# Kernel tuning notes

Hardware: AMD Instinct MI355X
Metric: run time of the kernel (lower is better)

## Reference

```python
import jax, jax.numpy as jnp
from jax import lax
import numpy as np

N_LAYER = 2
SEQ, BATCH, D = 4096, 32, 512


def setup_inputs() -> dict:
    key = jax.random.key(0)
    k1, k2, k3 = jax.random.split(key, 3)
    x = jax.random.normal(k1, (SEQ, BATCH, D), dtype=jnp.float32)
    # repo init: weight_ih ~ N(0, 0.01)
    W_ih = jax.random.normal(k2, (N_LAYER, D, D), dtype=jnp.float32) * 0.01
    # recurrent weight in [0,1) keeps the long ReLU recurrence bounded
    w_hh = jax.random.uniform(k3, (N_LAYER, D), dtype=jnp.float32)
    b_ih = jnp.zeros((N_LAYER, D), dtype=jnp.float32)
    return {"x": x, "W_ih": W_ih, "w_hh": w_hh, "b_ih": b_ih}


def _indrnn_layer(x, W, w, b):
    # x: (T, B, in), W: (H, in), w,b: (H,)
    proj = jnp.einsum('tbi,hi->tbh', x, W) + b  # one batched GEMM up front

    def step(h, p):
        h = jax.nn.relu(p + w * h)
        return h, h

    h0 = jnp.zeros((x.shape[1], W.shape[0]), dtype=x.dtype)
    hT, ys = lax.scan(step, h0, proj)
    return ys, hT


def reference(x, W_ih, w_hh, b_ih):
    hiddens = []
    out = x
    for l in range(W_ih.shape[0]):  # small fixed layer loop
        out, hT = _indrnn_layer(out, W_ih[l], w_hh[l], b_ih[l])
        hiddens.append(hT)
    h_n = jnp.stack(hiddens, axis=0)  # (n_layer, B, H)
    return out, h_n
```

## Files before the change

kernel.cpp:

```cpp
#include <hip/hip_runtime.h>

#define T_SEQ   4096
#define BATCH   32
#define DIM     512
#define MROWS   (T_SEQ * BATCH)
#define S_STRIDE (BATCH * DIM)
#define OUT_ELEMS ((size_t)T_SEQ * BATCH * DIM)
#define NCH     32
#define CLEN    (T_SEQ / NCH)
#define NCHAIN  (BATCH * DIM)
#define NWG     ((MROWS / 128) * (DIM / 128))

typedef __bf16 bf8_t __attribute__((ext_vector_type(8)));
typedef float  f4_t  __attribute__((ext_vector_type(4)));
typedef unsigned short u16x8 __attribute__((ext_vector_type(8)));
typedef __attribute__((address_space(1))) void gvoid_t;
typedef __attribute__((address_space(3))) void lvoid_t;

__device__ __forceinline__ unsigned short f2bf(float f) {
    unsigned int u = __float_as_uint(f);
    u += 0x7FFFu + ((u >> 16) & 1u);
    return (unsigned short)(u >> 16);
}
__device__ __forceinline__ float bf2f(unsigned short b) {
    return __uint_as_float(((unsigned int)b) << 16);
}

__global__ __launch_bounds__(256) void k_cvt(const float* __restrict__ in,
                                             unsigned short* __restrict__ out) {
    size_t i = ((size_t)blockIdx.x * 256 + threadIdx.x) * 8;
    float4 a = *reinterpret_cast<const float4*>(in + i);
    float4 b = *reinterpret_cast<const float4*>(in + i + 4);
    u16x8 o;
    o[0] = f2bf(a.x); o[1] = f2bf(a.y); o[2] = f2bf(a.z); o[3] = f2bf(a.w);
    o[4] = f2bf(b.x); o[5] = f2bf(b.y); o[6] = f2bf(b.z); o[7] = f2bf(b.w);
    *reinterpret_cast<u16x8*>(out + i) = o;
}

template <int AF32>
__global__ __launch_bounds__(256)
void k_gemm_bt(const void* __restrict__ Ap,
               const unsigned short* __restrict__ B,
               unsigned short* __restrict__ C) {
    __shared__ unsigned short As[128 * 32];
    __shared__ unsigned short Bs[128 * 32];

    const int tid  = threadIdx.x;
    const int lane = tid & 63;
    const int wv   = tid >> 6;
    const int wr   = wv >> 1;
    const int wc   = wv & 1;

    const int flat = blockIdx.x;
    const int s    = (flat & 7) * (NWG / 8) + (flat >> 3);
    const size_t gm = (size_t)(s >> 2) * 128;
    const int    gn = (s & 3) * 128;

    const int srow = tid >> 2;
    const int skk  = (tid & 3) * 8;

    f4_t acc[4][4] = {};

    const int l15 = lane & 15;
    const int lk  = (lane >> 4) * 8;

    for (int k0 = 0; k0 < 512; k0 += 32) {
#pragma unroll
        for (int i = 0; i < 2; ++i) {
            const unsigned short* gb = B + (size_t)(gn + i * 64 + srow) * 512 + k0 + skk;
            __builtin_amdgcn_global_load_lds((gvoid_t*)gb, (lvoid_t*)&Bs[i * 2048 + wv * 512], 16, 0, 0);
            if constexpr (AF32) {
                const float* ga = (const float*)Ap + (gm + (size_t)(i * 64 + srow)) * 512 + k0 + skk;
                float4 a0 = *reinterpret_cast<const float4*>(ga);
                float4 a1 = *reinterpret_cast<const float4*>(ga + 4);
                u16x8 o;
                o[0] = f2bf(a0.x); o[1] = f2bf(a0.y); o[2] = f2bf(a0.z); o[3] = f2bf(a0.w);
                o[4] = f2bf(a1.x); o[5] = f2bf(a1.y); o[6] = f2bf(a1.z); o[7] = f2bf(a1.w);
                *reinterpret_cast<u16x8*>(&As[i * 2048 + tid * 8]) = o;
            } else {
                const unsigned short* ga = (const unsigned short*)Ap + (gm + (size_t)(i * 64 + srow)) * 512 + k0 + skk;
                __builtin_amdgcn_global_load_lds((gvoid_t*)ga, (lvoid_t*)&As[i * 2048 + wv * 512], 16, 0, 0);
            }
        }
        __syncthreads();

        bf8_t af[4], bfz[4];
#pragma unroll
        for (int m = 0; m < 4; ++m)
            af[m] = *reinterpret_cast<const bf8_t*>(&As[(wr * 64 + m * 16 + l15) * 32 + lk]);
#pragma unroll
        for (int n = 0; n < 4; ++n)
            bfz[n] = *reinterpret_cast<const bf8_t*>(&Bs[(wc * 64 + n * 16 + l15) * 32 + lk]);
#pragma unroll
        for (int m = 0; m < 4; ++m)
#pragma unroll
            for (int n = 0; n < 4; ++n)
                acc[m][n] = __builtin_amdgcn_mfma_f32_16x16x32_bf16(af[m], bfz[n], acc[m][n], 0, 0, 0);
        __syncthreads();
    }

    const int crow0 = (lane >> 4) * 4;
#pragma unroll
    for (int m = 0; m < 4; ++m)
#pragma unroll
        for (int n = 0; n < 4; ++n) {
            const size_t row0 = gm + (size_t)(wr * 64 + m * 16 + crow0);
            const int    col  = gn + wc * 64 + n * 16 + l15;
#pragma unroll
            for (int r = 0; r < 4; ++r)
                C[(row0 + r) * 512 + col] = f2bf(acc[m][n][r]);
        }
}

__global__ __launch_bounds__(256)
void k_scan_p1(const unsigned short* __restrict__ q,
               const float* __restrict__ w_hh,
               const float* __restrict__ b_ih,
               float* __restrict__ Asum,
               float* __restrict__ Bsum) {
    const int g = (blockIdx.x & 63) * 256 + threadIdx.x;
    const int c = blockIdx.x >> 6;
    const float w  = w_hh[g & 511];
    const float bs = b_ih[g & 511];
    const unsigned short* p = q + (size_t)c * CLEN * S_STRIDE + g;

    float A = 0.f, Bv = 0.f;
    float s0[8], s1[8];
#pragma unroll
    for (int j = 0; j < 8; ++j) s0[j] = bf2f(p[(size_t)j * S_STRIDE]);
#pragma unroll
    for (int j = 0; j < 8; ++j) s1[j] = bf2f(p[(size_t)(8 + j) * S_STRIDE]);

    for (int j0 = 0; j0 < CLEN; j0 += 16) {
#pragma unroll
        for (int j = 0; j < 8; ++j) {
            float qv = s0[j] + bs;
            A  = fmaxf(fmaf(w, A, qv), 0.f);
            Bv = fmaf(w, Bv, qv);
        }
        if (j0 + 16 < CLEN) {
#pragma unroll
            for (int j = 0; j < 8; ++j) s0[j] = bf2f(p[(size_t)(j0 + 16 + j) * S_STRIDE]);
        }
#pragma unroll
        for (int j = 0; j < 8; ++j) {
            float qv = s1[j] + bs;
            A  = fmaxf(fmaf(w, A, qv), 0.f);
            Bv = fmaf(w, Bv, qv);
        }
        if (j0 + 24 < CLEN) {
#pragma unroll
            for (int j = 0; j < 8; ++j) s1[j] = bf2f(p[(size_t)(j0 + 24 + j) * S_STRIDE]);
        }
    }
    Asum[(size_t)c * NCHAIN + g] = A;
    Bsum[(size_t)c * NCHAIN + g] = Bv;
}

template <int MODE>
__global__ __launch_bounds__(256)
void k_scan_p2(const unsigned short* __restrict__ q,
               const float* __restrict__ w_hh,
               const float* __restrict__ b_ih,
               const float* __restrict__ Asum,
               const float* __restrict__ Bsum,
               float* __restrict__ of32,
               unsigned short* __restrict__ ob16,
               float* __restrict__ hT) {
    const int g = (blockIdx.x & 63) * 256 + threadIdx.x;
    const int c = blockIdx.x >> 6;
    const float w  = w_hh[g & 511];
    const float bs = b_ih[g & 511];

    float cw = w;
#pragma unroll
    for (int i = 0; i < 7; ++i) cw *= cw;
    float h = 0.f;
    for (int cc = 0; cc < c; ++cc)
        h = fmaxf(Asum[(size_t)cc * NCHAIN + g], fmaf(cw, h, Bsum[(size_t)cc * NCHAIN + g]));

    const size_t base = (size_t)c * CLEN * S_STRIDE + g;
    const unsigned short* p = q + base;

    float s0[8], s1[8];
#pragma unroll
    for (int j = 0; j < 8; ++j) s0[j] = bf2f(p[(size_t)j * S_STRIDE]);
#pragma unroll
    for (int j = 0; j < 8; ++j) s1[j] = bf2f(p[(size_t)(8 + j) * S_STRIDE]);

    for (int j0 = 0; j0 < CLEN; j0 += 16) {
#pragma unroll
        for (int j = 0; j < 8; ++j) {
            h = fmaxf(fmaf(w, h, s0[j] + bs), 0.f);
            const size_t idx = base + (size_t)(j0 + j) * S_STRIDE;
            if (MODE == 0) of32[idx] = h; else ob16[idx] = f2bf(h);
        }
        if (j0 + 16 < CLEN) {
#pragma unroll
            for (int j = 0; j < 8; ++j) s0[j] = bf2f(p[(size_t)(j0 + 16 + j) * S_STRIDE]);
        }
#pragma unroll
        for (int j = 0; j < 8; ++j) {
            h = fmaxf(fmaf(w, h, s1[j] + bs), 0.f);
            const size_t idx = base + (size_t)(j0 + 8 + j) * S_STRIDE;
            if (MODE == 0) of32[idx] = h; else ob16[idx] = f2bf(h);
        }
        if (j0 + 24 < CLEN) {
#pragma unroll
            for (int j = 0; j < 8; ++j) s1[j] = bf2f(p[(size_t)(j0 + 24 + j) * S_STRIDE]);
        }
    }
    if (c == NCH - 1) hT[g] = h;
}

extern "C" void kernel_launch(void* const* d_in, const int* in_sizes, int n_in,
                              void* d_out, int out_size, void* d_ws, size_t ws_size,
                              hipStream_t stream) {
    const float* x    = (const float*)d_in[0];
    const float* W_ih = (const float*)d_in[1];
    const float* w_hh = (const float*)d_in[2];
    const float* b_ih = (const float*)d_in[3];

    unsigned short* proj2 = (unsigned short*)d_ws;
    unsigned short* Wb    = proj2 + OUT_ELEMS;
    float* Asum = (float*)(Wb + 2 * 512 * 512);
    float* Bsum = Asum + (size_t)NCH * NCHAIN;

    unsigned short* proj1 = (unsigned short*)d_out;
    unsigned short* ys1   = proj1 + OUT_ELEMS;
    float* out = (float*)d_out;
    float* hT  = out + OUT_ELEMS;

    const int sgrid = 64 * NCH;

    k_cvt<<<524288 / 8 / 256, 256, 0, stream>>>(W_ih, Wb);
    k_gemm_bt<1><<<NWG, 256, 0, stream>>>(x, Wb, proj1);
    k_scan_p1<<<sgrid, 256, 0, stream>>>(proj1, w_hh, b_ih, Asum, Bsum);
    k_scan_p2<1><<<sgrid, 256, 0, stream>>>(proj1, w_hh, b_ih, Asum, Bsum,
                                            nullptr, ys1, hT);
    k_gemm_bt<0><<<NWG, 256, 0, stream>>>(ys1, Wb + 512 * 512, proj2);
    k_scan_p1<<<sgrid, 256, 0, stream>>>(proj2, w_hh + DIM, b_ih + DIM, Asum, Bsum);
    k_scan_p2<0><<<sgrid, 256, 0, stream>>>(proj2, w_hh + DIM, b_ih + DIM, Asum, Bsum,
                                            out, nullptr, hT + NCHAIN);
}
```

Baseline: 469.1 us.

## Keep weight tile in registers with persistent streaming GEMM over row chunks

```diff
diff --git a/kernel.cpp b/kernel.cpp
--- a/kernel.cpp
+++ b/kernel.cpp
@@ -9,7 +9,10 @@
 #define NCH     32
 #define CLEN    (T_SEQ / NCH)
 #define NCHAIN  (BATCH * DIM)
-#define NWG     ((MROWS / 128) * (DIM / 128))
+
+#define CHROWS  32
+#define NCHUNK  16
+#define LDSB    98304
 
 typedef __bf16 bf8_t __attribute__((ext_vector_type(8)));
 typedef float  f4_t  __attribute__((ext_vector_type(4)));
@@ -26,90 +29,134 @@
     return __uint_as_float(((unsigned int)b) << 16);
 }
 
-__global__ __launch_bounds__(256) void k_cvt(const float* __restrict__ in,
-                                             unsigned short* __restrict__ out) {
-    size_t i = ((size_t)blockIdx.x * 256 + threadIdx.x) * 8;
-    float4 a = *reinterpret_cast<const float4*>(in + i);
-    float4 b = *reinterpret_cast<const float4*>(in + i + 4);
-    u16x8 o;
-    o[0] = f2bf(a.x); o[1] = f2bf(a.y); o[2] = f2bf(a.z); o[3] = f2bf(a.w);
-    o[4] = f2bf(b.x); o[5] = f2bf(b.y); o[6] = f2bf(b.z); o[7] = f2bf(b.w);
-    *reinterpret_cast<u16x8*>(out + i) = o;
-}
+#define VMCn(n) asm volatile("s_waitcnt vmcnt(" #n ")" ::: "memory")
+#define LGKM0   asm volatile("s_waitcnt lgkmcnt(0)" ::: "memory")
 
 template <int AF32>
-__global__ __launch_bounds__(256)
-void k_gemm_bt(const void* __restrict__ Ap,
-               const unsigned short* __restrict__ B,
+__global__ __launch_bounds__(256, 1)
+void k_gemm_bs(const void* __restrict__ Ap,
+               const float* __restrict__ Bf,
                unsigned short* __restrict__ C) {
-    __shared__ unsigned short As[128 * 32];
-    __shared__ unsigned short Bs[128 * 32];
+    extern __shared__ unsigned short lds[];
 
     const int tid  = threadIdx.x;
     const int lane = tid & 63;
     const int wv   = tid >> 6;
-    const int wr   = wv >> 1;
-    const int wc   = wv & 1;
-
-    const int flat = blockIdx.x;
-    const int s    = (flat & 7) * (NWG / 8) + (flat >> 3);
-    const size_t gm = (size_t)(s >> 2) * 128;
-    const int    gn = (s & 3) * 128;
-
-    const int srow = tid >> 2;
-    const int skk  = (tid & 3) * 8;
-
-    f4_t acc[4][4] = {};
-
-    const int l15 = lane & 15;
-    const int lk  = (lane >> 4) * 8;
-
-    for (int k0 = 0; k0 < 512; k0 += 32) {
-#pragma unroll
-        for (int i = 0; i < 2; ++i) {
-            const unsigned short* gb = B + (size_t)(gn + i * 64 + srow) * 512 + k0 + skk;
-            __builtin_amdgcn_global_load_lds((gvoid_t*)gb, (lvoid_t*)&Bs[i * 2048 + wv * 512], 16, 0, 0);
-            if constexpr (AF32) {
-                const float* ga = (const float*)Ap + (gm + (size_t)(i * 64 + srow)) * 512 + k0 + skk;
-                float4 a0 = *reinterpret_cast<const float4*>(ga);
-                float4 a1 = *reinterpret_cast<const float4*>(ga + 4);
-                u16x8 o;
-                o[0] = f2bf(a0.x); o[1] = f2bf(a0.y); o[2] = f2bf(a0.z); o[3] = f2bf(a0.w);
-                o[4] = f2bf(a1.x); o[5] = f2bf(a1.y); o[6] = f2bf(a1.z); o[7] = f2bf(a1.w);
-                *reinterpret_cast<u16x8*>(&As[i * 2048 + tid * 8]) = o;
-            } else {
-                const unsigned short* ga = (const unsigned short*)Ap + (gm + (size_t)(i * 64 + srow)) * 512 + k0 + skk;
-                __builtin_amdgcn_global_load_lds((gvoid_t*)ga, (lvoid_t*)&As[i * 2048 + wv * 512], 16, 0, 0);
+    const int l15  = lane & 15;
+    const int l16  = lane >> 4;
+
+    const int d  = blockIdx.x;
+    const int p  = (d >> 4) * 8 + (d & 7);
+    const int nh = (d >> 3) & 1;
+    const size_t gm = (size_t)p * 512;
+    const int    nb = nh * 256 + wv * 64;
+
+    bf8_t bq[4][16];
+#pragma unroll
+    for (int n = 0; n < 4; ++n)
+#pragma unroll
+        for (int k = 0; k < 16; ++k) {
+            const float* bp = Bf + (size_t)(nb + n * 16 + l15) * 512 + k * 32 + l16 * 8;
+            float4 f0 = *reinterpret_cast<const float4*>(bp);
+            float4 f1 = *reinterpret_cast<const float4*>(bp + 4);
+            u16x8 o;
+            o[0] = f2bf(f0.x); o[1] = f2bf(f0.y); o[2] = f2bf(f0.z); o[3] = f2bf(f0.w);
+            o[4] = f2bf(f1.x); o[5] = f2bf(f1.y); o[6] = f2bf(f1.z); o[7] = f2bf(f1.w);
+            bq[n][k] = *reinterpret_cast<bf8_t*>(&o);
+        }
+
+    const unsigned short* Ab = (const unsigned short*)Ap;
+    const float*          Af = (const float*)Ap;
+
+    unsigned short* b0 = lds;
+    unsigned short* b1 = lds + 16384;
+    unsigned short* b2 = lds + 32768;
+
+    auto stage = [&](unsigned short* buf, int c) {
+#pragma unroll
+        for (int j = 0; j < 8; ++j) {
+            const int r = wv * 8 + j;
+            const unsigned short* src =
+                Ab + (gm + c * CHROWS + r) * 512 + ((lane ^ j) * 8);
+            __builtin_amdgcn_global_load_lds((gvoid_t*)src,
+                (lvoid_t*)&buf[r * 512], 16, 0, 0);
+        }
+    };
+    const int rr = tid >> 3, sg = tid & 7;
+    float4 P[16];
+    auto loadP = [&](int c) {
+        const float* src = Af + (gm + c * CHROWS + rr) * 512 + sg * 64;
+#pragma unroll
+        for (int q = 0; q < 16; ++q)
+            P[q] = *reinterpret_cast<const float4*>(src + q * 4);
+    };
+    auto writeP = [&](unsigned short* buf) {
+#pragma unroll
+        for (int i = 0; i < 8; ++i) {
+            u16x8 o;
+            o[0] = f2bf(P[2*i].x);   o[1] = f2bf(P[2*i].y);
+            o[2] = f2bf(P[2*i].z);   o[3] = f2bf(P[2*i].w);
+            o[4] = f2bf(P[2*i+1].x); o[5] = f2bf(P[2*i+1].y);
+            o[6] = f2bf(P[2*i+1].z); o[7] = f2bf(P[2*i+1].w);
+            const int s = sg * 8 + i;
+            *reinterpret_cast<u16x8*>(&buf[rr * 512 + ((s ^ (rr & 7)) * 8)]) = o;
+        }
+    };
+
+    if constexpr (AF32) {
+        loadP(0); VMCn(0); writeP(b0); LGKM0;
+        loadP(1);
+    } else {
+        stage(b0, 0); stage(b1, 1);
+        VMCn(8);
+    }
+    __builtin_amdgcn_s_barrier();
+
+    for (int c = 0; c < NCHUNK; ++c) {
+        if constexpr (!AF32) {
+            if (c + 2 < NCHUNK) stage(b2, c + 2);
+        }
+
+        f4_t acc[2][4] = {};
+#pragma unroll
+        for (int k = 0; k < 16; ++k) {
+            const int so = ((k * 4 + l16) ^ (l15 & 7)) * 8;
+            bf8_t a0 = *reinterpret_cast<const bf8_t*>(&b0[l15 * 512 + so]);
+            bf8_t a1 = *reinterpret_cast<const bf8_t*>(&b0[(16 + l15) * 512 + so]);
+#pragma unroll
+            for (int n = 0; n < 4; ++n) {
+                acc[0][n] = __builtin_amdgcn_mfma_f32_16x16x32_bf16(a0, bq[n][k], acc[0][n], 0, 0, 0);
+                acc[1][n] = __builtin_amdgcn_mfma_f32_16x16x32_bf16(a1, bq[n][k], acc[1][n], 0, 0, 0);
             }
         }
-        __syncthreads();
-
-        bf8_t af[4], bfz[4];
-#pragma unroll
-        for (int m = 0; m < 4; ++m)
-            af[m] = *reinterpret_cast<const bf8_t*>(&As[(wr * 64 + m * 16 + l15) * 32 + lk]);
-#pragma unroll
-        for (int n = 0; n < 4; ++n)
-            bfz[n] = *reinterpret_cast<const bf8_t*>(&Bs[(wc * 64 + n * 16 + l15) * 32 + lk]);
-#pragma unroll
-        for (int m = 0; m < 4; ++m)
-#pragma unroll
-            for (int n = 0; n < 4; ++n)
-                acc[m][n] = __builtin_amdgcn_mfma_f32_16x16x32_bf16(af[m], bfz[n], acc[m][n], 0, 0, 0);
-        __syncthreads();
-    }
-
-    const int crow0 = (lane >> 4) * 4;
-#pragma unroll
-    for (int m = 0; m < 4; ++m)
-#pragma unroll
-        for (int n = 0; n < 4; ++n) {
-            const size_t row0 = gm + (size_t)(wr * 64 + m * 16 + crow0);
-            const int    col  = gn + wc * 64 + n * 16 + l15;
-#pragma unroll
-            for (int r = 0; r < 4; ++r)
-                C[(row0 + r) * 512 + col] = f2bf(acc[m][n][r]);
-        }
+
+#pragma unroll
+        for (int m = 0; m < 2; ++m)
+#pragma unroll
+            for (int n = 0; n < 4; ++n) {
+                const size_t row0 = gm + c * CHROWS + m * 16 + l16 * 4;
+                const int    col  = nb + n * 16 + l15;
+#pragma unroll
+                for (int r = 0; r < 4; ++r)
+                    C[(row0 + r) * 512 + col] = f2bf(acc[m][n][r]);
+            }
+
+        if constexpr (AF32) {
+            if (c + 1 < NCHUNK) {
+                VMCn(32);
+                writeP(b1);
+                LGKM0;
+                if (c + 2 < NCHUNK) loadP(c + 2);
+                __builtin_amdgcn_s_barrier();
+            }
+            { unsigned short* t = b0; b0 = b1; b1 = t; }
+        } else {
+            if (c + 2 < NCHUNK)      { VMCn(40); }
+            else if (c + 1 < NCHUNK) { VMCn(32); }
+            if (c + 1 < NCHUNK) __builtin_amdgcn_s_barrier();
+            { unsigned short* t = b0; b0 = b1; b1 = b2; b2 = t; }
+        }
+    }
 }
 
 __global__ __launch_bounds__(256)
@@ -221,9 +268,13 @@
     const float* w_hh = (const float*)d_in[2];
     const float* b_ih = (const float*)d_in[3];
 
+    hipFuncSetAttribute(reinterpret_cast<const void*>(&k_gemm_bs<1>),
+                        hipFuncAttributeMaxDynamicSharedMemorySize, LDSB);
+    hipFuncSetAttribute(reinterpret_cast<const void*>(&k_gemm_bs<0>),
+                        hipFuncAttributeMaxDynamicSharedMemorySize, LDSB);
+
     unsigned short* proj2 = (unsigned short*)d_ws;
-    unsigned short* Wb    = proj2 + OUT_ELEMS;
-    float* Asum = (float*)(Wb + 2 * 512 * 512);
+    float* Asum = (float*)(proj2 + OUT_ELEMS);
     float* Bsum = Asum + (size_t)NCH * NCHAIN;
 
     unsigned short* proj1 = (unsigned short*)d_out;
@@ -233,12 +284,11 @@
 
     const int sgrid = 64 * NCH;
 
-    k_cvt<<<524288 / 8 / 256, 256, 0, stream>>>(W_ih, Wb);
-    k_gemm_bt<1><<<NWG, 256, 0, stream>>>(x, Wb, proj1);
+    k_gemm_bs<1><<<512, 256, LDSB, stream>>>(x, W_ih, proj1);
     k_scan_p1<<<sgrid, 256, 0, stream>>>(proj1, w_hh, b_ih, Asum, Bsum);
     k_scan_p2<1><<<sgrid, 256, 0, stream>>>(proj1, w_hh, b_ih, Asum, Bsum,
                                             nullptr, ys1, hT);
-    k_gemm_bt<0><<<NWG, 256, 0, stream>>>(ys1, Wb + 512 * 512, proj2);
+    k_gemm_bs<0><<<512, 256, LDSB, stream>>>(ys1, W_ih + 512 * 512, proj2);
     k_scan_p1<<<sgrid, 256, 0, stream>>>(proj2, w_hh + DIM, b_ih + DIM, Asum, Bsum);
     k_scan_p2<0><<<sgrid, 256, 0, stream>>>(proj2, w_hh + DIM, b_ih + DIM, Asum, Bsum,
                                             out, nullptr, hT + NCHAIN);
```

Measured after the change: 628.6 us. +34.0%, slower.
